# Kernel optimization log

Hardware: AMD Instinct MI355X
Metric: run time of the kernel (lower is better)

## Reference

```python
import jax, jax.numpy as jnp
import numpy as np

B, L, HEAD_IN, DIM = 16, 512, 4, 64
HEAD_OUT = 4


def setup_inputs() -> dict:
    key = jax.random.key(0)
    k1, k2 = jax.random.split(key)
    inp = jax.random.normal(k1, (B, L, HEAD_IN, DIM), dtype=jnp.float32)
    # one (dim x dim) 'general' attention weight per (head_out, head_in) pair
    W = jax.random.normal(k2, (HEAD_OUT, HEAD_IN, DIM, DIM), dtype=jnp.float32) / np.sqrt(DIM)
    return {"inp": inp, "W": W}


def reference(inp, W):
    # inp: [b, l, j(head_in), d]; W: [o(head_out), j, d, e]
    b, l, j, d = inp.shape
    scale = 1.0 / jnp.sqrt(jnp.asarray(d, inp.dtype))
    # q_ij = x_j @ W_ij  -> [o, j, b, l, e]
    q = jnp.einsum('bljd,ojde->ojble', inp, W)
    # scores_ij = q_ij @ x_j^T / sqrt(d) -> [o, j, b, l, m]
    scores = jnp.einsum('ojble,bmje->ojblm', q, inp) * scale
    attn = jax.nn.softmax(scores, axis=-1)          # [o, j, b, l, m]
    ctx = jnp.einsum('ojblm,bmjd->ojbld', attn, inp)  # [o, j, b, l, d]
    out = jnp.mean(ctx, axis=1)                      # mean over head_in -> [o, b, l, d]
    out = jnp.transpose(out, (1, 2, 0, 3))           # [b, l, head_out, d]
    return out, attn
```

## Files before the change

kernel.cpp:

```cpp
#include <hip/hip_runtime.h>
#include <stdint.h>


typedef __bf16 bf16x8 __attribute__((ext_vector_type(8)));
typedef float  f32x4  __attribute__((ext_vector_type(4)));

#define XRM_OFF 0
#define XCM_OFF 65536
#define WT_OFF  132096
#define QB_OFF  141312
#define ACH_OFF 132096
#define LDS_BYTES 159744

__device__ __forceinline__ unsigned short f2bf(float f) {
    unsigned int u = __builtin_bit_cast(unsigned int, f);
    u += 0x7fffu + ((u >> 16) & 1u);
    return (unsigned short)(u >> 16);
}

__global__ __launch_bounds__(512, 2) void convattn_kernel(
    const float* __restrict__ inp,
    const float* __restrict__ Wg,
    float* __restrict__ out)
{
    extern __shared__ __align__(16) char smem[];

    const int tid  = threadIdx.x;
    const int wave = tid >> 6;
    const int lane = tid & 63;
    const int g    = lane >> 4;
    const int ln   = lane & 15;

    const int bid = blockIdx.x;
    const int b  = bid & 15;
    const int o  = (bid >> 4) & 3;
    const int lt = bid >> 6;

    float* attn_out = out + (size_t)2097152;

    f32x4 acc_c[4];
    #pragma unroll
    for (int i = 0; i < 4; ++i) { f32x4 z = {0.f,0.f,0.f,0.f}; acc_c[i] = z; }

    for (int j = 0; j < 4; ++j) {
        __syncthreads();

        {
            const int mrow = tid >> 4;
            const int e0   = (tid & 15) << 2;
            #pragma unroll
            for (int it = 0; it < 16; ++it) {
                const int m = it * 32 + mrow;
                const float4 v = *(const float4*)(inp + (((size_t)b * 512 + m) * 4 + j) * 64 + e0);
                const unsigned short b0 = f2bf(v.x), b1 = f2bf(v.y),
                                     b2 = f2bf(v.z), b3 = f2bf(v.w);
                char* p = smem + XRM_OFF + m * 128 + (((e0 >> 3) ^ (m & 7)) * 16) + (e0 & 7) * 2;
                *(unsigned int*)(p)     = (unsigned int)b0 | ((unsigned int)b1 << 16);
                *(unsigned int*)(p + 4) = (unsigned int)b2 | ((unsigned int)b3 << 16);
                *(unsigned short*)(smem + XCM_OFF + (e0 + 0) * 1040 + m * 2) = b0;
                *(unsigned short*)(smem + XCM_OFF + (e0 + 1) * 1040 + m * 2) = b1;
                *(unsigned short*)(smem + XCM_OFF + (e0 + 2) * 1040 + m * 2) = b2;
                *(unsigned short*)(smem + XCM_OFF + (e0 + 3) * 1040 + m * 2) = b3;
            }
            #pragma unroll
            for (int it = 0; it < 2; ++it) {
                const int d = it * 32 + mrow;
                const float4 v = *(const float4*)(Wg + (((size_t)o * 4 + j) * 64 + d) * 64 + e0);
                *(unsigned short*)(smem + WT_OFF + (e0 + 0) * 144 + d * 2) = f2bf(v.x);
                *(unsigned short*)(smem + WT_OFF + (e0 + 1) * 144 + d * 2) = f2bf(v.y);
                *(unsigned short*)(smem + WT_OFF + (e0 + 2) * 144 + d * 2) = f2bf(v.z);
                *(unsigned short*)(smem + WT_OFF + (e0 + 3) * 144 + d * 2) = f2bf(v.w);
            }
        }
        __syncthreads();

        {
            const int lr = lt * 128 + wave * 16 + ln;
            const bf16x8 a0 = *(const bf16x8*)(smem + XRM_OFF + lr * 128 + (((0 + g) ^ (lr & 7)) * 16));
            const bf16x8 a1 = *(const bf16x8*)(smem + XRM_OFF + lr * 128 + (((4 + g) ^ (lr & 7)) * 16));
            char* qb = smem + QB_OFF + wave * 2304;
            #pragma unroll
            for (int et = 0; et < 4; ++et) {
                const int e = et * 16 + ln;
                const bf16x8 bw0 = *(const bf16x8*)(smem + WT_OFF + e * 144 + g * 16);
                const bf16x8 bw1 = *(const bf16x8*)(smem + WT_OFF + e * 144 + 64 + g * 16);
                f32x4 t = {0.f,0.f,0.f,0.f};
                t = __builtin_amdgcn_mfma_f32_16x16x32_bf16(a0, bw0, t, 0, 0, 0);
                t = __builtin_amdgcn_mfma_f32_16x16x32_bf16(a1, bw1, t, 0, 0, 0);
                #pragma unroll
                for (int r = 0; r < 4; ++r)
                    *(unsigned short*)(qb + (g * 4 + r) * 144 + e * 2) = f2bf(t[r]);
            }
        }
        __syncthreads();

        bf16x8 aq0, aq1;
        {
            const char* qb = smem + QB_OFF + wave * 2304;
            aq0 = *(const bf16x8*)(qb + ln * 144 + g * 16);
            aq1 = *(const bf16x8*)(qb + ln * 144 + 64 + g * 16);
        }

        f32x4 accs[32];
        #pragma unroll
        for (int mt = 0; mt < 32; ++mt) {
            const int m = mt * 16 + ln;
            const bf16x8 xb0 = *(const bf16x8*)(smem + XRM_OFF + m * 128 + (((0 + g) ^ (m & 7)) * 16));
            const bf16x8 xb1 = *(const bf16x8*)(smem + XRM_OFF + m * 128 + (((4 + g) ^ (m & 7)) * 16));
            f32x4 t = {0.f,0.f,0.f,0.f};
            t = __builtin_amdgcn_mfma_f32_16x16x32_bf16(aq0, xb0, t, 0, 0, 0);
            t = __builtin_amdgcn_mfma_f32_16x16x32_bf16(aq1, xb1, t, 0, 0, 0);
            accs[mt] = t;
        }

        float mx[4], inv[4];
        #pragma unroll
        for (int r = 0; r < 4; ++r) {
            float m0 = -3.402823466e+38f;
            #pragma unroll
            for (int mt = 0; mt < 32; ++mt) m0 = fmaxf(m0, accs[mt][r]);
            #pragma unroll
            for (int s = 1; s < 16; s <<= 1) m0 = fmaxf(m0, __shfl_xor(m0, s, 64));
            mx[r] = m0;
        }
        #pragma unroll
        for (int r = 0; r < 4; ++r) {
            float s0 = 0.f;
            #pragma unroll
            for (int mt = 0; mt < 32; ++mt) {
                const float e = __expf((accs[mt][r] - mx[r]) * 0.125f);
                accs[mt][r] = e;
                s0 += e;
            }
            #pragma unroll
            for (int s = 1; s < 16; s <<= 1) s0 += __shfl_xor(s0, s, 64);
            inv[r] = 1.0f / s0;
        }
        #pragma unroll
        for (int mt = 0; mt < 32; ++mt) {
            #pragma unroll
            for (int r = 0; r < 4; ++r) accs[mt][r] *= inv[r];
        }

        {
            const size_t abase = (size_t)((o * 4 + j) * 16 + b) * 262144;
            const int l0 = lt * 128 + wave * 16 + g * 4;
            #pragma unroll
            for (int r = 0; r < 4; ++r) {
                float* rowp = attn_out + abase + (size_t)(l0 + r) * 512 + ln;
                #pragma unroll
                for (int mt = 0; mt < 32; ++mt)
                    __builtin_nontemporal_store(accs[mt][r], rowp + mt * 16);
            }
        }

        {
            char* ach = smem + ACH_OFF + wave * 2304;
            for (int c = 0; c < 8; ++c) {
                #pragma unroll
                for (int t4 = 0; t4 < 4; ++t4) {
                    const int mt = c * 4 + t4;
                    #pragma unroll
                    for (int r = 0; r < 4; ++r)
                        *(unsigned short*)(ach + (g * 4 + r) * 144 + (t4 * 16 + ln) * 2) = f2bf(accs[mt][r]);
                }
                __syncthreads();
                const bf16x8 pa0 = *(const bf16x8*)(ach + ln * 144 + g * 16);
                const bf16x8 pa1 = *(const bf16x8*)(ach + ln * 144 + 64 + g * 16);
                #pragma unroll
                for (int dt = 0; dt < 4; ++dt) {
                    const int d = dt * 16 + ln;
                    const bf16x8 xb0 = *(const bf16x8*)(smem + XCM_OFF + d * 1040 + c * 128 + g * 16);
                    const bf16x8 xb1 = *(const bf16x8*)(smem + XCM_OFF + d * 1040 + c * 128 + 64 + g * 16);
                    acc_c[dt] = __builtin_amdgcn_mfma_f32_16x16x32_bf16(pa0, xb0, acc_c[dt], 0, 0, 0);
                    acc_c[dt] = __builtin_amdgcn_mfma_f32_16x16x32_bf16(pa1, xb1, acc_c[dt], 0, 0, 0);
                }
            }
        }
    }

    {
        const int l0 = lt * 128 + wave * 16 + g * 4;
        #pragma unroll
        for (int dt = 0; dt < 4; ++dt) {
            #pragma unroll
            for (int r = 0; r < 4; ++r) {
                const int l = l0 + r;
                out[(((size_t)b * 512 + l) * 4 + o) * 64 + dt * 16 + ln] = acc_c[dt][r] * 0.25f;
            }
        }
    }
}

extern "C" void kernel_launch(void* const* d_in, const int* in_sizes, int n_in,
                              void* d_out, int out_size, void* d_ws, size_t ws_size,
                              hipStream_t stream) {
    const float* inp = (const float*)d_in[0];
    const float* Wg  = (const float*)d_in[1];
    float* out = (float*)d_out;

    (void)hipFuncSetAttribute((const void*)convattn_kernel,
                              hipFuncAttributeMaxDynamicSharedMemorySize, LDS_BYTES);

    convattn_kernel<<<dim3(256), dim3(512), LDS_BYTES, stream>>>(inp, Wg, out);
}
```

Before: 393.3 us.

## Recompute scores in two passes, pass softmax via shuffles, vectorize attn stores

The score tile is now computed twice, once for the row max and once for exp and sum, so only packed bf16 exponentials are kept in registers instead of 32 fp32 accumulators. The softmax probabilities reach the P·V MFMA B operand through cross-lane shuffles instead of a staged LDS buffer with a block barrier per chunk. Attention and output stores are transposed through a small per-wave LDS scratch so each lane writes float4 vectors. The transposed X layout is changed to an XOR-swizzled, unpadded format and loads are widened. The trade is double the QK MFMA work and attention values rounded through bf16 before normalization, in exchange for lower register pressure, fewer barriers and wider global writes.

Measured after the change: 357.3 us. 1.1x faster.

```diff
diff --git a/kernel.cpp b/kernel.cpp
--- a/kernel.cpp
+++ b/kernel.cpp
@@ -4,19 +4,22 @@
 
 typedef __bf16 bf16x8 __attribute__((ext_vector_type(8)));
 typedef float  f32x4  __attribute__((ext_vector_type(4)));
+typedef unsigned int u32;
+typedef u32 u32x4 __attribute__((ext_vector_type(4)));
 
 #define XRM_OFF 0
 #define XCM_OFF 65536
-#define WT_OFF  132096
-#define QB_OFF  141312
-#define ACH_OFF 132096
-#define LDS_BYTES 159744
-
-__device__ __forceinline__ unsigned short f2bf(float f) {
-    unsigned int u = __builtin_bit_cast(unsigned int, f);
+#define WT_OFF  131072
+#define QB_OFF  140288
+#define LDS_BYTES 158720
+
+static __device__ __forceinline__ u32 f2bf(float f) {
+    u32 u = __builtin_bit_cast(u32, f);
     u += 0x7fffu + ((u >> 16) & 1u);
-    return (unsigned short)(u >> 16);
+    return u >> 16;
 }
+static __device__ __forceinline__ float bflo2f(u32 p) { return __builtin_bit_cast(float, p << 16); }
+static __device__ __forceinline__ float bfhi2f(u32 p) { return __builtin_bit_cast(float, p & 0xffff0000u); }
 
 __global__ __launch_bounds__(512, 2) void convattn_kernel(
     const float* __restrict__ inp,
@@ -24,171 +27,178 @@
     float* __restrict__ out)
 {
     extern __shared__ __align__(16) char smem[];
-
     const int tid  = threadIdx.x;
     const int wave = tid >> 6;
     const int lane = tid & 63;
     const int g    = lane >> 4;
     const int ln   = lane & 15;
+    const int rl   = lane >> 2;
+    const int rq   = lane & 3;
 
     const int bid = blockIdx.x;
     const int b  = bid & 15;
     const int o  = (bid >> 4) & 3;
     const int lt = bid >> 6;
+    const int l0 = lt * 128 + wave * 16;
 
     float* attn_out = out + (size_t)2097152;
+    char* qb = smem + QB_OFF + wave * 2304;
 
     f32x4 acc_c[4];
     #pragma unroll
     for (int i = 0; i < 4; ++i) { f32x4 z = {0.f,0.f,0.f,0.f}; acc_c[i] = z; }
 
+    #pragma unroll 1
     for (int j = 0; j < 4; ++j) {
         __syncthreads();
 
         {
-            const int mrow = tid >> 4;
-            const int e0   = (tid & 15) << 2;
-            #pragma unroll
-            for (int it = 0; it < 16; ++it) {
-                const int m = it * 32 + mrow;
-                const float4 v = *(const float4*)(inp + (((size_t)b * 512 + m) * 4 + j) * 64 + e0);
-                const unsigned short b0 = f2bf(v.x), b1 = f2bf(v.y),
-                                     b2 = f2bf(v.z), b3 = f2bf(v.w);
-                char* p = smem + XRM_OFF + m * 128 + (((e0 >> 3) ^ (m & 7)) * 16) + (e0 & 7) * 2;
-                *(unsigned int*)(p)     = (unsigned int)b0 | ((unsigned int)b1 << 16);
-                *(unsigned int*)(p + 4) = (unsigned int)b2 | ((unsigned int)b3 << 16);
-                *(unsigned short*)(smem + XCM_OFF + (e0 + 0) * 1040 + m * 2) = b0;
-                *(unsigned short*)(smem + XCM_OFF + (e0 + 1) * 1040 + m * 2) = b1;
-                *(unsigned short*)(smem + XCM_OFF + (e0 + 2) * 1040 + m * 2) = b2;
-                *(unsigned short*)(smem + XCM_OFF + (e0 + 3) * 1040 + m * 2) = b3;
+            const int q = tid & 15, p = tid >> 4;
+            const int e0 = q << 2;
+            #pragma unroll
+            for (int it = 0; it < 8; ++it) {
+                const int m0 = it * 64 + p * 2;
+                const float* src = inp + (((size_t)b * 512 + m0) * 4 + j) * 64 + e0;
+                const float4 va = *(const float4*)src;
+                const float4 vb = *(const float4*)(src + 256);
+                const u32 pa0 = f2bf(va.x), pa1 = f2bf(va.y), pa2 = f2bf(va.z), pa3 = f2bf(va.w);
+                const u32 pb0 = f2bf(vb.x), pb1 = f2bf(vb.y), pb2 = f2bf(vb.z), pb3 = f2bf(vb.w);
+                {
+                    uint2 w0; w0.x = pa0 | (pa1 << 16); w0.y = pa2 | (pa3 << 16);
+                    *(uint2*)(smem + XRM_OFF + m0 * 128 + (((q >> 1) ^ (m0 & 7)) * 16) + ((q & 1) * 8)) = w0;
+                    uint2 w1; w1.x = pb0 | (pb1 << 16); w1.y = pb2 | (pb3 << 16);
+                    *(uint2*)(smem + XRM_OFF + (m0 + 1) * 128 + (((q >> 1) ^ ((m0 + 1) & 7)) * 16) + ((q & 1) * 8)) = w1;
+                }
+                const u32 pc[4] = { pa0 | (pb0 << 16), pa1 | (pb1 << 16),
+                                    pa2 | (pb2 << 16), pa3 | (pb3 << 16) };
+                #pragma unroll
+                for (int c = 0; c < 4; ++c) {
+                    const int d = e0 + c;
+                    *(u32*)(smem + XCM_OFF + d * 1024 + (((m0 >> 3) ^ ((d >> 2) & 7)) * 16) + (m0 & 7) * 2) = pc[c];
+                }
             }
             #pragma unroll
             for (int it = 0; it < 2; ++it) {
-                const int d = it * 32 + mrow;
-                const float4 v = *(const float4*)(Wg + (((size_t)o * 4 + j) * 64 + d) * 64 + e0);
-                *(unsigned short*)(smem + WT_OFF + (e0 + 0) * 144 + d * 2) = f2bf(v.x);
-                *(unsigned short*)(smem + WT_OFF + (e0 + 1) * 144 + d * 2) = f2bf(v.y);
-                *(unsigned short*)(smem + WT_OFF + (e0 + 2) * 144 + d * 2) = f2bf(v.z);
-                *(unsigned short*)(smem + WT_OFF + (e0 + 3) * 144 + d * 2) = f2bf(v.w);
+                const int d = it * 32 + p;
+                const float4 wv = *(const float4*)(Wg + (((size_t)o * 4 + j) * 64 + d) * 64 + e0);
+                *(unsigned short*)(smem + WT_OFF + (e0 + 0) * 144 + d * 2) = (unsigned short)f2bf(wv.x);
+                *(unsigned short*)(smem + WT_OFF + (e0 + 1) * 144 + d * 2) = (unsigned short)f2bf(wv.y);
+                *(unsigned short*)(smem + WT_OFF + (e0 + 2) * 144 + d * 2) = (unsigned short)f2bf(wv.z);
+                *(unsigned short*)(smem + WT_OFF + (e0 + 3) * 144 + d * 2) = (unsigned short)f2bf(wv.w);
             }
         }
         __syncthreads();
 
         {
-            const int lr = lt * 128 + wave * 16 + ln;
-            const bf16x8 a0 = *(const bf16x8*)(smem + XRM_OFF + lr * 128 + (((0 + g) ^ (lr & 7)) * 16));
-            const bf16x8 a1 = *(const bf16x8*)(smem + XRM_OFF + lr * 128 + (((4 + g) ^ (lr & 7)) * 16));
-            char* qb = smem + QB_OFF + wave * 2304;
+            const int lq = l0 + ln;
+            const bf16x8 aq0 = *(const bf16x8*)(smem + XRM_OFF + lq * 128 + (((0 + g) ^ (lq & 7)) * 16));
+            const bf16x8 aq1 = *(const bf16x8*)(smem + XRM_OFF + lq * 128 + (((4 + g) ^ (lq & 7)) * 16));
             #pragma unroll
             for (int et = 0; et < 4; ++et) {
                 const int e = et * 16 + ln;
                 const bf16x8 bw0 = *(const bf16x8*)(smem + WT_OFF + e * 144 + g * 16);
                 const bf16x8 bw1 = *(const bf16x8*)(smem + WT_OFF + e * 144 + 64 + g * 16);
                 f32x4 t = {0.f,0.f,0.f,0.f};
-                t = __builtin_amdgcn_mfma_f32_16x16x32_bf16(a0, bw0, t, 0, 0, 0);
-                t = __builtin_amdgcn_mfma_f32_16x16x32_bf16(a1, bw1, t, 0, 0, 0);
+                t = __builtin_amdgcn_mfma_f32_16x16x32_bf16(aq0, bw0, t, 0, 0, 0);
+                t = __builtin_amdgcn_mfma_f32_16x16x32_bf16(aq1, bw1, t, 0, 0, 0);
                 #pragma unroll
                 for (int r = 0; r < 4; ++r)
-                    *(unsigned short*)(qb + (g * 4 + r) * 144 + e * 2) = f2bf(t[r]);
-            }
-        }
-        __syncthreads();
-
-        bf16x8 aq0, aq1;
-        {
-            const char* qb = smem + QB_OFF + wave * 2304;
-            aq0 = *(const bf16x8*)(qb + ln * 144 + g * 16);
-            aq1 = *(const bf16x8*)(qb + ln * 144 + 64 + g * 16);
-        }
-
-        f32x4 accs[32];
+                    *(unsigned short*)(qb + (g * 4 + r) * 144 + e * 2) = (unsigned short)f2bf(t[r]);
+            }
+        }
+        const bf16x8 bq0 = *(const bf16x8*)(qb + ln * 144 + g * 16);
+        const bf16x8 bq1 = *(const bf16x8*)(qb + ln * 144 + 64 + g * 16);
+
+        float mx = -3.402823466e+38f;
         #pragma unroll
         for (int mt = 0; mt < 32; ++mt) {
             const int m = mt * 16 + ln;
-            const bf16x8 xb0 = *(const bf16x8*)(smem + XRM_OFF + m * 128 + (((0 + g) ^ (m & 7)) * 16));
-            const bf16x8 xb1 = *(const bf16x8*)(smem + XRM_OFF + m * 128 + (((4 + g) ^ (m & 7)) * 16));
+            const bf16x8 ax0 = *(const bf16x8*)(smem + XRM_OFF + m * 128 + (((0 + g) ^ (m & 7)) * 16));
+            const bf16x8 ax1 = *(const bf16x8*)(smem + XRM_OFF + m * 128 + (((4 + g) ^ (m & 7)) * 16));
             f32x4 t = {0.f,0.f,0.f,0.f};
-            t = __builtin_amdgcn_mfma_f32_16x16x32_bf16(aq0, xb0, t, 0, 0, 0);
-            t = __builtin_amdgcn_mfma_f32_16x16x32_bf16(aq1, xb1, t, 0, 0, 0);
-            accs[mt] = t;
-        }
-
-        float mx[4], inv[4];
-        #pragma unroll
-        for (int r = 0; r < 4; ++r) {
-            float m0 = -3.402823466e+38f;
-            #pragma unroll
-            for (int mt = 0; mt < 32; ++mt) m0 = fmaxf(m0, accs[mt][r]);
-            #pragma unroll
-            for (int s = 1; s < 16; s <<= 1) m0 = fmaxf(m0, __shfl_xor(m0, s, 64));
-            mx[r] = m0;
-        }
-        #pragma unroll
-        for (int r = 0; r < 4; ++r) {
-            float s0 = 0.f;
-            #pragma unroll
-            for (int mt = 0; mt < 32; ++mt) {
-                const float e = __expf((accs[mt][r] - mx[r]) * 0.125f);
-                accs[mt][r] = e;
-                s0 += e;
-            }
-            #pragma unroll
-            for (int s = 1; s < 16; s <<= 1) s0 += __shfl_xor(s0, s, 64);
-            inv[r] = 1.0f / s0;
-        }
+            t = __builtin_amdgcn_mfma_f32_16x16x32_bf16(ax0, bq0, t, 0, 0, 0);
+            t = __builtin_amdgcn_mfma_f32_16x16x32_bf16(ax1, bq1, t, 0, 0, 0);
+            mx = fmaxf(mx, fmaxf(fmaxf(t[0], t[1]), fmaxf(t[2], t[3])));
+        }
+        mx = fmaxf(mx, __shfl_xor(mx, 16, 64));
+        mx = fmaxf(mx, __shfl_xor(mx, 32, 64));
+
+        float sum = 0.f;
+        u32 sLo[32], sHi[32];
         #pragma unroll
         for (int mt = 0; mt < 32; ++mt) {
-            #pragma unroll
-            for (int r = 0; r < 4; ++r) accs[mt][r] *= inv[r];
-        }
-
-        {
-            const size_t abase = (size_t)((o * 4 + j) * 16 + b) * 262144;
-            const int l0 = lt * 128 + wave * 16 + g * 4;
-            #pragma unroll
-            for (int r = 0; r < 4; ++r) {
-                float* rowp = attn_out + abase + (size_t)(l0 + r) * 512 + ln;
-                #pragma unroll
-                for (int mt = 0; mt < 32; ++mt)
-                    __builtin_nontemporal_store(accs[mt][r], rowp + mt * 16);
-            }
-        }
-
-        {
-            char* ach = smem + ACH_OFF + wave * 2304;
-            for (int c = 0; c < 8; ++c) {
-                #pragma unroll
-                for (int t4 = 0; t4 < 4; ++t4) {
-                    const int mt = c * 4 + t4;
-                    #pragma unroll
-                    for (int r = 0; r < 4; ++r)
-                        *(unsigned short*)(ach + (g * 4 + r) * 144 + (t4 * 16 + ln) * 2) = f2bf(accs[mt][r]);
-                }
-                __syncthreads();
-                const bf16x8 pa0 = *(const bf16x8*)(ach + ln * 144 + g * 16);
-                const bf16x8 pa1 = *(const bf16x8*)(ach + ln * 144 + 64 + g * 16);
-                #pragma unroll
-                for (int dt = 0; dt < 4; ++dt) {
-                    const int d = dt * 16 + ln;
-                    const bf16x8 xb0 = *(const bf16x8*)(smem + XCM_OFF + d * 1040 + c * 128 + g * 16);
-                    const bf16x8 xb1 = *(const bf16x8*)(smem + XCM_OFF + d * 1040 + c * 128 + 64 + g * 16);
-                    acc_c[dt] = __builtin_amdgcn_mfma_f32_16x16x32_bf16(pa0, xb0, acc_c[dt], 0, 0, 0);
-                    acc_c[dt] = __builtin_amdgcn_mfma_f32_16x16x32_bf16(pa1, xb1, acc_c[dt], 0, 0, 0);
-                }
+            const int m = mt * 16 + ln;
+            const bf16x8 ax0 = *(const bf16x8*)(smem + XRM_OFF + m * 128 + (((0 + g) ^ (m & 7)) * 16));
+            const bf16x8 ax1 = *(const bf16x8*)(smem + XRM_OFF + m * 128 + (((4 + g) ^ (m & 7)) * 16));
+            f32x4 t = {0.f,0.f,0.f,0.f};
+            t = __builtin_amdgcn_mfma_f32_16x16x32_bf16(ax0, bq0, t, 0, 0, 0);
+            t = __builtin_amdgcn_mfma_f32_16x16x32_bf16(ax1, bq1, t, 0, 0, 0);
+            const float e0v = __expf((t[0] - mx) * 0.125f);
+            const float e1v = __expf((t[1] - mx) * 0.125f);
+            const float e2v = __expf((t[2] - mx) * 0.125f);
+            const float e3v = __expf((t[3] - mx) * 0.125f);
+            sum += (e0v + e1v) + (e2v + e3v);
+            sLo[mt] = f2bf(e0v) | (f2bf(e1v) << 16);
+            sHi[mt] = f2bf(e2v) | (f2bf(e3v) << 16);
+        }
+        sum += __shfl_xor(sum, 16, 64);
+        sum += __shfl_xor(sum, 32, 64);
+        const float inv = 1.0f / sum;
+
+        const size_t abase = ((size_t)((o * 4 + j) * 16 + b)) * 262144 + (size_t)l0 * 512;
+        const int srcLo = ((g & 1) << 5) + ln;
+        const int srcHi = srcLo + 16;
+        #pragma unroll
+        for (int ch = 0; ch < 16; ++ch) {
+            u32 pLo[2], pHi[2];
+            #pragma unroll
+            for (int s = 0; s < 2; ++s) {
+                const int mt = ch * 2 + s;
+                const float a0v = bflo2f(sLo[mt]) * inv;
+                const float a1v = bfhi2f(sLo[mt]) * inv;
+                const float a2v = bflo2f(sHi[mt]) * inv;
+                const float a3v = bfhi2f(sHi[mt]) * inv;
+                *(float*)(qb + ln * 80 + (g * 4 + 0) * 4) = a0v;
+                *(float*)(qb + ln * 80 + (g * 4 + 1) * 4) = a1v;
+                *(float*)(qb + ln * 80 + (g * 4 + 2) * 4) = a2v;
+                *(float*)(qb + ln * 80 + (g * 4 + 3) * 4) = a3v;
+                const f32x4 rv = *(const f32x4*)(qb + rl * 80 + rq * 16);
+                __builtin_nontemporal_store(rv,
+                    (f32x4*)(attn_out + abase + (size_t)rl * 512 + mt * 16 + rq * 4));
+                pLo[s] = f2bf(a0v) | (f2bf(a1v) << 16);
+                pHi[s] = f2bf(a2v) | (f2bf(a3v) << 16);
+            }
+            const u32 a0s = (u32)__shfl((int)pLo[0], srcLo, 64);
+            const u32 a1s = (u32)__shfl((int)pHi[0], srcLo, 64);
+            const u32 a2s = (u32)__shfl((int)pLo[0], srcHi, 64);
+            const u32 a3s = (u32)__shfl((int)pHi[0], srcHi, 64);
+            const u32 b0s = (u32)__shfl((int)pLo[1], srcLo, 64);
+            const u32 b1s = (u32)__shfl((int)pHi[1], srcLo, 64);
+            const u32 b2s = (u32)__shfl((int)pLo[1], srcHi, 64);
+            const u32 b3s = (u32)__shfl((int)pHi[1], srcHi, 64);
+            const bool hi = (g >= 2);
+            const u32 dw0 = hi ? b0s : a0s;
+            const u32 dw1 = hi ? b1s : a1s;
+            const u32 dw2 = hi ? b2s : a2s;
+            const u32 dw3 = hi ? b3s : a3s;
+            const bf16x8 bfrag = __builtin_bit_cast(bf16x8, (u32x4){dw0, dw1, dw2, dw3});
+            #pragma unroll
+            for (int dt = 0; dt < 4; ++dt) {
+                const int d = dt * 16 + ln;
+                const bf16x8 ax = *(const bf16x8*)(smem + XCM_OFF + d * 1024 +
+                                   (((ch * 4 + g) ^ ((d >> 2) & 7)) * 16));
+                acc_c[dt] = __builtin_amdgcn_mfma_f32_16x16x32_bf16(ax, bfrag, acc_c[dt], 0, 0, 0);
             }
         }
     }
 
-    {
-        const int l0 = lt * 128 + wave * 16 + g * 4;
-        #pragma unroll
-        for (int dt = 0; dt < 4; ++dt) {
-            #pragma unroll
-            for (int r = 0; r < 4; ++r) {
-                const int l = l0 + r;
-                out[(((size_t)b * 512 + l) * 4 + o) * 64 + dt * 16 + ln] = acc_c[dt][r] * 0.25f;
-            }
-        }
+    #pragma unroll
+    for (int dt = 0; dt < 4; ++dt) {
+        #pragma unroll
+        for (int r = 0; r < 4; ++r)
+            *(float*)(qb + ln * 80 + (g * 4 + r) * 4) = acc_c[dt][r] * 0.25f;
+        const f32x4 rv = *(const f32x4*)(qb + rl * 80 + rq * 16);
+        *(f32x4*)(out + (((size_t)b * 512 + (l0 + rl)) * 4 + o) * 64 + dt * 16 + rq * 4) = rv;
     }
 }
 
@@ -198,9 +208,7 @@
     const float* inp = (const float*)d_in[0];
     const float* Wg  = (const float*)d_in[1];
     float* out = (float*)d_out;
-
     (void)hipFuncSetAttribute((const void*)convattn_kernel,
                               hipFuncAttributeMaxDynamicSharedMemorySize, LDS_BYTES);
-
     convattn_kernel<<<dim3(256), dim3(512), LDS_BYTES, stream>>>(inp, Wg, out);
 }
```
